# Optimization experiments

Hardware: AMD Instinct MI355X
Metric: run time of the kernel (lower is better)

The kernel has to match this reference:

```python
import jax, jax.numpy as jnp
import numpy as np

B, T, E, H = 1, 4096, 1024, 16
HD = E // H  # 64
SCALE = 8.0 / HD  # scaling='d' per Tensor Programs V


def setup_inputs() -> dict:
    key = jax.random.key(0)
    ks = jax.random.split(key, 7)
    s = 1.0 / np.sqrt(E)
    return {
        "q": jax.random.normal(ks[0], (B, T, E), jnp.float32),
        "k": jax.random.normal(ks[1], (B, T, E), jnp.float32),
        "v": jax.random.normal(ks[2], (B, T, E), jnp.float32),
        "Wq": jax.random.normal(ks[3], (E, E), jnp.float32) * s,
        "Wk": jax.random.normal(ks[4], (E, E), jnp.float32) * s,
        "Wv": jax.random.normal(ks[5], (E, E), jnp.float32) * s,
        "Wo": jax.random.normal(ks[6], (E, E), jnp.float32) * s,
    }


def reference(q, k, v, Wq, Wk, Wv, Wo):
    # bias-free linear projections (nn.Linear: y = x @ W.T)
    qp = q @ Wq.T
    kp = k @ Wk.T
    vp = v @ Wv.T
    # b t (h d) -> b h t d
    qh = qp.reshape(B, T, H, HD).transpose(0, 2, 1, 3)
    kh = kp.reshape(B, T, H, HD).transpose(0, 2, 1, 3)
    vh = vp.reshape(B, T, H, HD).transpose(0, 2, 1, 3)
    scores = jnp.einsum('bhqd,bhkd->bhqk', qh, kh) * SCALE
    # causal mask: positions k > q masked with -inf
    causal = jnp.tril(jnp.ones((T, T), dtype=bool))
    scores = jnp.where(causal[None, None], scores, -jnp.inf)
    probs = jax.nn.softmax(scores, axis=-1)
    out = jnp.einsum('bhqk,bhkd->bhqd', probs, vh)
    # b h t d -> b t (h d)
    out = out.transpose(0, 2, 1, 3).reshape(B, T, E)
    return out @ Wo.T
```

## Files before the change

kernel.cpp:

```cpp
#include <hip/hip_runtime.h>
#include <hip/hip_bf16.h>

#define T_DIM 4096
#define E_DIM 1024
#define H_DIM 16
#define HD_DIM 64
#define LOG2E_F 1.4426950408889634f
#define QSCALE_F (0.125f * LOG2E_F)

typedef __bf16 bf16_t;
typedef __bf16 bf16x8 __attribute__((ext_vector_type(8)));
typedef __bf16 bf16x4 __attribute__((ext_vector_type(4)));
typedef float  f32x4  __attribute__((ext_vector_type(4)));

__device__ inline void stage8(bf16_t* dst, const float* src) {
  const f32x4* s4 = (const f32x4*)src;
  f32x4 a = s4[0], b = s4[1];
  bf16x8 o;
  o[0] = (bf16_t)a[0]; o[1] = (bf16_t)a[1]; o[2] = (bf16_t)a[2]; o[3] = (bf16_t)a[3];
  o[4] = (bf16_t)b[0]; o[5] = (bf16_t)b[1]; o[6] = (bf16_t)b[2]; o[7] = (bf16_t)b[3];
  *(bf16x8*)dst = o;
}
__device__ inline void stage8(bf16_t* dst, const bf16_t* src) {
  *(bf16x8*)dst = *(const bf16x8*)src;
}

__device__ inline void gld_lds16(const bf16_t* g, bf16_t* l) {
  __builtin_amdgcn_global_load_lds(
      (const __attribute__((address_space(1))) unsigned int*)g,
      (__attribute__((address_space(3))) unsigned int*)l, 16, 0, 0);
}

__device__ inline float fexp2(float x) {
  float r;
  asm("v_exp_f32 %0, %1" : "=v"(r) : "v"(x));
  return r;
}

__device__ inline void block_sync() {
  asm volatile("" ::: "memory");
  __builtin_amdgcn_s_barrier();
  asm volatile("" ::: "memory");
}

__global__ __launch_bounds__(256) void cvt_all(
    const float* __restrict__ q, const float* __restrict__ k, const float* __restrict__ v,
    const float* __restrict__ Wq, const float* __restrict__ Wk,
    const float* __restrict__ Wv, const float* __restrict__ Wo,
    bf16_t* qb, bf16_t* kb, bf16_t* vb,
    bf16_t* Wqb, bf16_t* Wkb, bf16_t* Wvb, bf16_t* Wob) {
  for (int u = blockIdx.x * 256 + threadIdx.x; u < 2097152; u += gridDim.x * 256) {
    const float* s; bf16_t* d; int i;
    if (u < 1572864) {
      int seg = u >> 19, off = u & 524287;
      s = seg == 0 ? q : (seg == 1 ? k : v);
      d = seg == 0 ? qb : (seg == 1 ? kb : vb);
      i = off;
    } else {
      int w = u - 1572864;
      int seg = w >> 17, off = w & 131071;
      s = seg == 0 ? Wq : seg == 1 ? Wk : seg == 2 ? Wv : Wo;
      d = seg == 0 ? Wqb : seg == 1 ? Wkb : seg == 2 ? Wvb : Wob;
      i = off;
    }
    stage8(d + (size_t)i * 8, s + (size_t)i * 8);
  }
}

template <int MF, int NF, typename TC>
__device__ __forceinline__ void gemm_body(const bf16_t* __restrict__ A,
                                          const bf16_t* __restrict__ B,
                                          TC* __restrict__ C,
                                          int ldC, int bm, int bn, float cs) {
  constexpr int BM = 32 * MF, BN = 32 * NF;
  __shared__ alignas(16) bf16_t As[BM][64];
  __shared__ alignas(16) bf16_t Bs[BN][64];
  const int tid  = threadIdx.x;
  const int lane = tid & 63, w = tid >> 6;
  const int g = lane >> 4, l15 = lane & 15;
  const int wr = w >> 1, wc = w & 1;

  f32x4 acc[MF][NF] = {};

  for (int kt = 0; kt < 1024; kt += 64) {
    if (kt) __syncthreads();
#pragma unroll
    for (int p = 0; p < MF; ++p) {
      int s = p * 256 + tid;
      int row = s >> 3, c = s & 7;
      int cg = c ^ (row & 7);
      gld_lds16(&A[(size_t)(bm + row) * 1024 + kt + cg * 8], &As[0][0] + s * 8);
    }
#pragma unroll
    for (int p = 0; p < NF; ++p) {
      int s = p * 256 + tid;
      int row = s >> 3, c = s & 7;
      int cg = c ^ (row & 7);
      gld_lds16(&B[(size_t)(bn + row) * 1024 + kt + cg * 8], &Bs[0][0] + s * 8);
    }
    asm volatile("s_waitcnt vmcnt(0)" ::: "memory");
    __syncthreads();

#pragma unroll
    for (int hh = 0; hh < 2; ++hh) {
      bf16x8 af[MF], bfr[NF];
#pragma unroll
      for (int m = 0; m < MF; ++m) {
        int row = wr * (16 * MF) + m * 16 + l15;
        af[m] = *(const bf16x8*)(&As[0][0] + row * 64 + (((hh * 4 + g) ^ (row & 7)) * 8));
      }
#pragma unroll
      for (int n = 0; n < NF; ++n) {
        int row = wc * (16 * NF) + n * 16 + l15;
        bfr[n] = *(const bf16x8*)(&Bs[0][0] + row * 64 + (((hh * 4 + g) ^ (row & 7)) * 8));
      }
#pragma unroll
      for (int m = 0; m < MF; ++m)
#pragma unroll
        for (int n = 0; n < NF; ++n)
          acc[m][n] = __builtin_amdgcn_mfma_f32_16x16x32_bf16(af[m], bfr[n], acc[m][n], 0, 0, 0);
    }
  }

#pragma unroll
  for (int m = 0; m < MF; ++m)
#pragma unroll
    for (int n = 0; n < NF; ++n)
#pragma unroll
      for (int r = 0; r < 4; ++r) {
        int row = bm + wr * (16 * MF) + m * 16 + g * 4 + r;
        int col = bn + wc * (16 * NF) + n * 16 + l15;
        C[(size_t)row * ldC + col] = (TC)(acc[m][n][r] * cs);
      }
}

__global__ __launch_bounds__(256) void proj_qkv(
    const bf16_t* __restrict__ qb, const bf16_t* __restrict__ kb,
    const bf16_t* __restrict__ vb,
    const bf16_t* __restrict__ Wqb, const bf16_t* __restrict__ Wkb,
    const bf16_t* __restrict__ Wvb,
    bf16_t* Qp, bf16_t* Kp, bf16_t* Vt) {
  const int bid = blockIdx.x;
  const int which = bid >> 8, t = bid & 255;
  const bf16_t *A, *B; bf16_t* C; int ldC, bm, bn; float cs;
  if (which == 0) {
    A = qb;  B = Wqb; C = Qp; ldC = 1024;
    bm = (t >> 3) * 128; bn = (t & 7) * 128; cs = QSCALE_F;
  } else if (which == 1) {
    A = kb;  B = Wkb; C = Kp; ldC = 1024;
    bm = (t >> 3) * 128; bn = (t & 7) * 128; cs = 1.0f;
  } else {
    A = Wvb; B = vb;  C = Vt; ldC = 4096;
    bm = (t >> 5) * 128; bn = (t & 31) * 128; cs = 1.0f;
  }
  gemm_body<4, 4, bf16_t>(A, B, C, ldC, bm, bn, cs);
}

__global__ __launch_bounds__(256) void gemm_fin(const bf16_t* __restrict__ A,
                                                const bf16_t* __restrict__ B,
                                                float* __restrict__ C) {
  gemm_body<2, 4, float>(A, B, C, 1024, blockIdx.y * 64, blockIdx.x * 128, 1.0f);
}

template <typename TA, typename TB, typename TC>
__global__ __launch_bounds__(256) void gemm_bt(const TA* __restrict__ A,
                                               const TB* __restrict__ B,
                                               TC* __restrict__ C,
                                               int M, int N, int K, float cscale) {
  __shared__ alignas(16) bf16_t As[128][40];
  __shared__ alignas(16) bf16_t Bs[128][40];
  const int tid  = threadIdx.x;
  const int lane = tid & 63, w = tid >> 6;
  const int g = lane >> 4, l15 = lane & 15;
  const int wr = w >> 1, wc = w & 1;
  const int bm = blockIdx.y * 128, bn = blockIdx.x * 128;

  f32x4 acc[4][4] = {};

  for (int kt = 0; kt < K; kt += 32) {
    __syncthreads();
#pragma unroll
    for (int i = 0; i < 2; ++i) {
      int vv  = tid + i * 256;
      int row = vv >> 2, c8 = (vv & 3) * 8;
      stage8(&As[row][c8], &A[(size_t)(bm + row) * K + kt + c8]);
      stage8(&Bs[row][c8], &B[(size_t)(bn + row) * K + kt + c8]);
    }
    __syncthreads();

    bf16x8 af[4], bfr[4];
#pragma unroll
    for (int m = 0; m < 4; ++m)
      af[m] = *(const bf16x8*)&As[wr * 64 + m * 16 + l15][g * 8];
#pragma unroll
    for (int n = 0; n < 4; ++n)
      bfr[n] = *(const bf16x8*)&Bs[wc * 64 + n * 16 + l15][g * 8];
#pragma unroll
    for (int m = 0; m < 4; ++m)
#pragma unroll
      for (int n = 0; n < 4; ++n)
        acc[m][n] = __builtin_amdgcn_mfma_f32_16x16x32_bf16(af[m], bfr[n], acc[m][n], 0, 0, 0);
  }

#pragma unroll
  for (int m = 0; m < 4; ++m)
#pragma unroll
    for (int n = 0; n < 4; ++n)
#pragma unroll
      for (int r = 0; r < 4; ++r) {
        int row = bm + wr * 64 + m * 16 + g * 4 + r;
        int col = bn + wc * 64 + n * 16 + l15;
        C[(size_t)row * N + col] = (TC)(acc[m][n][r] * cscale);
      }
}

__global__ __launch_bounds__(256) void attn_fwd(const bf16_t* __restrict__ Qp,
                                                const bf16_t* __restrict__ Kp,
                                                const bf16_t* __restrict__ Vt,
                                                bf16_t* __restrict__ Oattn) {
  const int bid = blockIdx.x;
  const int h  = bid & 15;
  const int ii = bid >> 4;
  const int tid = threadIdx.x, lane = tid & 63, w = tid >> 6;
  const int g = lane >> 4, l15 = lane & 15;

  __shared__ alignas(16) bf16_t Ks[2][64][64];
  __shared__ alignas(16) bf16_t Vs[3][64][64];
  __shared__ alignas(16) bf16_t Plds[4][16][72];

  const int row0 = tid >> 3, c0 = tid & 7;
  const int cgo = (c0 ^ (row0 & 7)) * 8;
  const bf16_t* srcK0 = Kp + (size_t)row0 * E_DIM + h * 64 + cgo;
  const bf16_t* srcK1 = srcK0 + (size_t)32 * E_DIM;
  const bf16_t* srcV0 = Vt + (size_t)(h * 64 + row0) * T_DIM + cgo;
  const bf16_t* srcV1 = srcV0 + (size_t)32 * T_DIM;
  bf16_t* KsAll = &Ks[0][0][0];
  bf16_t* VsAll = &Vs[0][0][0];
  const size_t KADV = (size_t)64 * E_DIM;

  auto issue = [&](int t) {
    bf16_t* kd = KsAll + (t & 1) * 4096;
    bf16_t* vd = VsAll + (t % 3) * 4096;
    gld_lds16(srcK0 + (size_t)t * KADV, kd + tid * 8);
    gld_lds16(srcK1 + (size_t)t * KADV, kd + (256 + tid) * 8);
    gld_lds16(srcV0 + (size_t)t * 64,   vd + tid * 8);
    gld_lds16(srcV1 + (size_t)t * 64,   vd + (256 + tid) * 8);
  };

  f32x4 acc[4];
  float m_s, l_p;

  auto pv = [&](int t) {
    const char* Vb = (const char*)(VsAll + (t % 3) * 4096);
    bf16x8 pf0 = *(const bf16x8*)&Plds[w][l15][g * 8];
    bf16x8 pf1 = *(const bf16x8*)&Plds[w][l15][32 + g * 8];
#pragma unroll
    for (int c = 0; c < 4; ++c) {
      const int vr = c * 16 + l15;
      const char* rp = Vb + vr * 128;
      const int sw = (vr & 7) << 4;
      bf16x8 v0 = *(const bf16x8*)(rp + ((g * 16) ^ sw));
      bf16x8 v1 = *(const bf16x8*)(rp + ((64 + g * 16) ^ sw));
      acc[c] = __builtin_amdgcn_mfma_f32_16x16x32_bf16(v0, pf0, acc[c], 0, 0, 0);
      acc[c] = __builtin_amdgcn_mfma_f32_16x16x32_bf16(v1, pf1, acc[c], 0, 0, 0);
    }
  };

  for (int pass = 0; pass < 2; ++pass) {
    const int qi = pass ? ii : 63 - ii;
    const int qrow = qi * 64 + w * 16;
    const int nt = qi + 1;

    bf16x8 qf[2];
    {
      const bf16_t* qp = &Qp[(size_t)(qrow + l15) * E_DIM + h * 64 + g * 8];
      qf[0] = *(const bf16x8*)qp;
      qf[1] = *(const bf16x8*)(qp + 32);
    }
#pragma unroll
    for (int c = 0; c < 4; ++c)
#pragma unroll
      for (int r = 0; r < 4; ++r) acc[c][r] = 0.f;
    m_s = -1e30f; l_p = 0.f;

    if (pass) block_sync();
    issue(0);

    for (int j = 0; j < nt; ++j) {
      asm volatile("s_waitcnt vmcnt(0)" ::: "memory");
      block_sync();
      if (j + 1 < nt) issue(j + 1);

      __builtin_amdgcn_s_setprio(1);
      if (j > 0) pv(j - 1);

      const char* Kb = (const char*)(KsAll + (j & 1) * 4096);
      f32x4 s[4] = {};
#pragma unroll
      for (int j16 = 0; j16 < 4; ++j16) {
        const int r0 = j16 * 16 + l15;
        const char* rp = Kb + r0 * 128;
        const int sw = (r0 & 7) << 4;
        bf16x8 k0 = *(const bf16x8*)(rp + ((g * 16) ^ sw));
        bf16x8 k1 = *(const bf16x8*)(rp + ((64 + g * 16) ^ sw));
        s[j16] = __builtin_amdgcn_mfma_f32_16x16x32_bf16(k0, qf[0], s[j16], 0, 0, 0);
        s[j16] = __builtin_amdgcn_mfma_f32_16x16x32_bf16(k1, qf[1], s[j16], 0, 0, 0);
      }
      __builtin_amdgcn_s_setprio(0);

      if (j == nt - 1) {
        const int kb = j * 64;
#pragma unroll
        for (int j16 = 0; j16 < 4; ++j16)
#pragma unroll
          for (int r = 0; r < 4; ++r)
            if (kb + j16 * 16 + g * 4 + r > qrow + l15) s[j16][r] = -1e30f;
      }

      float pmax = s[0][0];
#pragma unroll
      for (int j16 = 0; j16 < 4; ++j16)
#pragma unroll
        for (int r = 0; r < 4; ++r) pmax = fmaxf(pmax, s[j16][r]);

      if (!__all(pmax <= m_s + 11.0f)) {
        float rm = fmaxf(pmax, __shfl_xor(pmax, 16));
        rm = fmaxf(rm, __shfl_xor(rm, 32));
        float mn = fmaxf(m_s, rm);
        float sc = fexp2(m_s - mn);
        m_s = mn;
        l_p *= sc;
#pragma unroll
        for (int c = 0; c < 4; ++c)
#pragma unroll
          for (int r = 0; r < 4; ++r) acc[c][r] *= sc;
      }

      float ps = 0.f;
#pragma unroll
      for (int j16 = 0; j16 < 4; ++j16)
#pragma unroll
        for (int r = 0; r < 4; ++r) {
          s[j16][r] = fexp2(s[j16][r] - m_s);
          ps += s[j16][r];
        }
      l_p += ps;

#pragma unroll
      for (int j16 = 0; j16 < 4; ++j16) {
        bf16x4 pk;
        pk[0] = (bf16_t)s[j16][0]; pk[1] = (bf16_t)s[j16][1];
        pk[2] = (bf16_t)s[j16][2]; pk[3] = (bf16_t)s[j16][3];
        *(bf16x4*)&Plds[w][l15][j16 * 16 + g * 4] = pk;
      }
    }

    pv(nt - 1);

    float lt = l_p;
    lt += __shfl_xor(lt, 16);
    lt += __shfl_xor(lt, 32);
    const float inv = 1.0f / lt;
#pragma unroll
    for (int c = 0; c < 4; ++c) {
      bf16x4 o;
#pragma unroll
      for (int r = 0; r < 4; ++r) o[r] = (bf16_t)(acc[c][r] * inv);
      *(bf16x4*)&Oattn[(size_t)(qrow + l15) * E_DIM + h * 64 + c * 16 + g * 4] = o;
    }
  }
}

extern "C" void kernel_launch(void* const* d_in, const int* in_sizes, int n_in,
                              void* d_out, int out_size, void* d_ws, size_t ws_size,
                              hipStream_t stream) {
  const float* q  = (const float*)d_in[0];
  const float* k  = (const float*)d_in[1];
  const float* v  = (const float*)d_in[2];
  const float* Wq = (const float*)d_in[3];
  const float* Wk = (const float*)d_in[4];
  const float* Wv = (const float*)d_in[5];
  const float* Wo = (const float*)d_in[6];
  float* out = (float*)d_out;

  const size_t TE = (size_t)T_DIM * E_DIM;
  const size_t EE = (size_t)E_DIM * E_DIM;
  dim3 blk(256);

  if (ws_size >= (size_t)56 * 1024 * 1024) {
    bf16_t* qb  = (bf16_t*)d_ws;
    bf16_t* kb  = qb + TE;
    bf16_t* vb  = kb + TE;
    bf16_t* Wqb = vb + TE;
    bf16_t* Wkb = Wqb + EE;
    bf16_t* Wvb = Wkb + EE;
    bf16_t* Wob = Wvb + EE;
    bf16_t* Qp  = Wob + EE;
    bf16_t* Kp  = Qp + TE;
    bf16_t* Vt  = Kp + TE;
    bf16_t* Oa  = qb;

    cvt_all<<<2048, blk, 0, stream>>>(q, k, v, Wq, Wk, Wv, Wo,
                                      qb, kb, vb, Wqb, Wkb, Wvb, Wob);
    proj_qkv<<<dim3(768), blk, 0, stream>>>(qb, kb, vb, Wqb, Wkb, Wvb, Qp, Kp, Vt);
    attn_fwd<<<dim3(512), blk, 0, stream>>>(Qp, Kp, Vt, Oa);
    gemm_fin<<<dim3(8, 64), blk, 0, stream>>>(Oa, Wob, out);
  } else {
    bf16_t* Qp = (bf16_t*)d_ws;
    bf16_t* Kp = Qp + TE;
    bf16_t* Vt = Kp + TE;
    bf16_t* Oa = Vt + TE;
    gemm_bt<float, float, bf16_t><<<dim3(8, 32), blk, 0, stream>>>(q, Wq, Qp, T_DIM, E_DIM, E_DIM, QSCALE_F);
    gemm_bt<float, float, bf16_t><<<dim3(8, 32), blk, 0, stream>>>(k, Wk, Kp, T_DIM, E_DIM, E_DIM, 1.0f);
    gemm_bt<float, float, bf16_t><<<dim3(32, 8), blk, 0, stream>>>(Wv, v, Vt, E_DIM, T_DIM, E_DIM, 1.0f);
    attn_fwd<<<dim3(512), blk, 0, stream>>>(Qp, Kp, Vt, Oa);
    gemm_bt<bf16_t, float, float><<<dim3(8, 32), blk, 0, stream>>>(Oa, Wo, out, T_DIM, E_DIM, E_DIM, 1.0f);
  }
}
```

Before: 131.6 us.

## Process two adjacent 64-row query tiles per block sharing each K/V tile

Each wave now carries two query row groups, 64 rows apart, within a 128-row block tile. Every K/V tile staged in shared memory feeds both groups' QK and PV MFMAs, which halves global K/V traffic per query row and doubles the independent MFMA work per sync. This replaces the old scheme that ran two mirrored 64-row tiles one after the other for load balance. The new mapping gives blocks uneven work (2 to 64 iterations), only partly offset by launching heavy blocks first. It also adds a fully masked extra tile for the first group and raises register pressure.

New measurement: 144.2 us. +9.6%, slower.

```diff
diff --git a/kernel.cpp b/kernel.cpp
--- a/kernel.cpp
+++ b/kernel.cpp
@@ -219,14 +219,27 @@
                                                 const bf16_t* __restrict__ Vt,
                                                 bf16_t* __restrict__ Oattn) {
   const int bid = blockIdx.x;
-  const int h  = bid & 15;
-  const int ii = bid >> 4;
+  const int h   = bid & 15;
+  const int idx = bid >> 4;
+  const int qi  = idx < 16 ? 31 - idx : idx - 16;
   const int tid = threadIdx.x, lane = tid & 63, w = tid >> 6;
   const int g = lane >> 4, l15 = lane & 15;
+  const int qrow_a = qi * 128 + w * 16;
+  const int qrow_b = qrow_a + 64;
 
   __shared__ alignas(16) bf16_t Ks[2][64][64];
   __shared__ alignas(16) bf16_t Vs[3][64][64];
-  __shared__ alignas(16) bf16_t Plds[4][16][72];
+  __shared__ alignas(16) bf16_t Plds[2][4][16][72];
+
+  bf16x8 qfa[2], qfb[2];
+  {
+    const bf16_t* qp = &Qp[(size_t)(qrow_a + l15) * E_DIM + h * 64 + g * 8];
+    qfa[0] = *(const bf16x8*)qp;
+    qfa[1] = *(const bf16x8*)(qp + 32);
+    const bf16_t* qp2 = qp + (size_t)64 * E_DIM;
+    qfb[0] = *(const bf16x8*)qp2;
+    qfb[1] = *(const bf16x8*)(qp2 + 32);
+  }
 
   const int row0 = tid >> 3, c0 = tid & 7;
   const int cgo = (c0 ^ (row0 & 7)) * 8;
@@ -237,6 +250,7 @@
   bf16_t* KsAll = &Ks[0][0][0];
   bf16_t* VsAll = &Vs[0][0][0];
   const size_t KADV = (size_t)64 * E_DIM;
+  const int nt = 2 * qi + 2;
 
   auto issue = [&](int t) {
     bf16_t* kd = KsAll + (t & 1) * 4096;
@@ -247,13 +261,16 @@
     gld_lds16(srcV1 + (size_t)t * 64,   vd + (256 + tid) * 8);
   };
 
-  f32x4 acc[4];
-  float m_s, l_p;
+  f32x4 acca[4] = {}, accb[4] = {};
+  float m_a = -1e30f, l_a = 0.f;
+  float m_b = -1e30f, l_b = 0.f;
 
   auto pv = [&](int t) {
     const char* Vb = (const char*)(VsAll + (t % 3) * 4096);
-    bf16x8 pf0 = *(const bf16x8*)&Plds[w][l15][g * 8];
-    bf16x8 pf1 = *(const bf16x8*)&Plds[w][l15][32 + g * 8];
+    bf16x8 pa0 = *(const bf16x8*)&Plds[0][w][l15][g * 8];
+    bf16x8 pa1 = *(const bf16x8*)&Plds[0][w][l15][32 + g * 8];
+    bf16x8 pb0 = *(const bf16x8*)&Plds[1][w][l15][g * 8];
+    bf16x8 pb1 = *(const bf16x8*)&Plds[1][w][l15][32 + g * 8];
 #pragma unroll
     for (int c = 0; c < 4; ++c) {
       const int vr = c * 16 + l15;
@@ -261,113 +278,115 @@
       const int sw = (vr & 7) << 4;
       bf16x8 v0 = *(const bf16x8*)(rp + ((g * 16) ^ sw));
       bf16x8 v1 = *(const bf16x8*)(rp + ((64 + g * 16) ^ sw));
-      acc[c] = __builtin_amdgcn_mfma_f32_16x16x32_bf16(v0, pf0, acc[c], 0, 0, 0);
-      acc[c] = __builtin_amdgcn_mfma_f32_16x16x32_bf16(v1, pf1, acc[c], 0, 0, 0);
+      acca[c] = __builtin_amdgcn_mfma_f32_16x16x32_bf16(v0, pa0, acca[c], 0, 0, 0);
+      acca[c] = __builtin_amdgcn_mfma_f32_16x16x32_bf16(v1, pa1, acca[c], 0, 0, 0);
+      accb[c] = __builtin_amdgcn_mfma_f32_16x16x32_bf16(v0, pb0, accb[c], 0, 0, 0);
+      accb[c] = __builtin_amdgcn_mfma_f32_16x16x32_bf16(v1, pb1, accb[c], 0, 0, 0);
     }
   };
 
-  for (int pass = 0; pass < 2; ++pass) {
-    const int qi = pass ? ii : 63 - ii;
-    const int qrow = qi * 64 + w * 16;
-    const int nt = qi + 1;
-
-    bf16x8 qf[2];
-    {
-      const bf16_t* qp = &Qp[(size_t)(qrow + l15) * E_DIM + h * 64 + g * 8];
-      qf[0] = *(const bf16x8*)qp;
-      qf[1] = *(const bf16x8*)(qp + 32);
-    }
-#pragma unroll
-    for (int c = 0; c < 4; ++c)
-#pragma unroll
-      for (int r = 0; r < 4; ++r) acc[c][r] = 0.f;
-    m_s = -1e30f; l_p = 0.f;
-
-    if (pass) block_sync();
-    issue(0);
-
-    for (int j = 0; j < nt; ++j) {
-      asm volatile("s_waitcnt vmcnt(0)" ::: "memory");
-      block_sync();
-      if (j + 1 < nt) issue(j + 1);
-
-      __builtin_amdgcn_s_setprio(1);
-      if (j > 0) pv(j - 1);
-
-      const char* Kb = (const char*)(KsAll + (j & 1) * 4096);
-      f32x4 s[4] = {};
-#pragma unroll
-      for (int j16 = 0; j16 < 4; ++j16) {
-        const int r0 = j16 * 16 + l15;
-        const char* rp = Kb + r0 * 128;
-        const int sw = (r0 & 7) << 4;
-        bf16x8 k0 = *(const bf16x8*)(rp + ((g * 16) ^ sw));
-        bf16x8 k1 = *(const bf16x8*)(rp + ((64 + g * 16) ^ sw));
-        s[j16] = __builtin_amdgcn_mfma_f32_16x16x32_bf16(k0, qf[0], s[j16], 0, 0, 0);
-        s[j16] = __builtin_amdgcn_mfma_f32_16x16x32_bf16(k1, qf[1], s[j16], 0, 0, 0);
+  auto softmax_p = [&](f32x4 (&s)[4], float& m_s, float& l_p, f32x4 (&acc)[4],
+                       int grp) {
+    float pmax = s[0][0];
+#pragma unroll
+    for (int j16 = 0; j16 < 4; ++j16)
+#pragma unroll
+      for (int r = 0; r < 4; ++r) pmax = fmaxf(pmax, s[j16][r]);
+
+    if (!__all(pmax <= m_s + 11.0f)) {
+      float rm = fmaxf(pmax, __shfl_xor(pmax, 16));
+      rm = fmaxf(rm, __shfl_xor(rm, 32));
+      float mn = fmaxf(m_s, rm);
+      float sc = fexp2(m_s - mn);
+      m_s = mn;
+      l_p *= sc;
+#pragma unroll
+      for (int c = 0; c < 4; ++c)
+#pragma unroll
+        for (int r = 0; r < 4; ++r) acc[c][r] *= sc;
+    }
+
+    float ps = 0.f;
+#pragma unroll
+    for (int j16 = 0; j16 < 4; ++j16)
+#pragma unroll
+      for (int r = 0; r < 4; ++r) {
+        s[j16][r] = fexp2(s[j16][r] - m_s);
+        ps += s[j16][r];
       }
-      __builtin_amdgcn_s_setprio(0);
-
-      if (j == nt - 1) {
-        const int kb = j * 64;
-#pragma unroll
-        for (int j16 = 0; j16 < 4; ++j16)
-#pragma unroll
-          for (int r = 0; r < 4; ++r)
-            if (kb + j16 * 16 + g * 4 + r > qrow + l15) s[j16][r] = -1e30f;
-      }
-
-      float pmax = s[0][0];
+    l_p += ps;
+
+#pragma unroll
+    for (int j16 = 0; j16 < 4; ++j16) {
+      bf16x4 pk;
+      pk[0] = (bf16_t)s[j16][0]; pk[1] = (bf16_t)s[j16][1];
+      pk[2] = (bf16_t)s[j16][2]; pk[3] = (bf16_t)s[j16][3];
+      *(bf16x4*)&Plds[grp][w][l15][j16 * 16 + g * 4] = pk;
+    }
+  };
+
+  issue(0);
+
+  for (int j = 0; j < nt; ++j) {
+    asm volatile("s_waitcnt vmcnt(0)" ::: "memory");
+    block_sync();
+    if (j + 1 < nt) issue(j + 1);
+
+    __builtin_amdgcn_s_setprio(1);
+    if (j > 0) pv(j - 1);
+
+    const char* Kb = (const char*)(KsAll + (j & 1) * 4096);
+    f32x4 sa[4] = {}, sb[4] = {};
+#pragma unroll
+    for (int j16 = 0; j16 < 4; ++j16) {
+      const int r0 = j16 * 16 + l15;
+      const char* rp = Kb + r0 * 128;
+      const int sw = (r0 & 7) << 4;
+      bf16x8 k0 = *(const bf16x8*)(rp + ((g * 16) ^ sw));
+      bf16x8 k1 = *(const bf16x8*)(rp + ((64 + g * 16) ^ sw));
+      sa[j16] = __builtin_amdgcn_mfma_f32_16x16x32_bf16(k0, qfa[0], sa[j16], 0, 0, 0);
+      sa[j16] = __builtin_amdgcn_mfma_f32_16x16x32_bf16(k1, qfa[1], sa[j16], 0, 0, 0);
+      sb[j16] = __builtin_amdgcn_mfma_f32_16x16x32_bf16(k0, qfb[0], sb[j16], 0, 0, 0);
+      sb[j16] = __builtin_amdgcn_mfma_f32_16x16x32_bf16(k1, qfb[1], sb[j16], 0, 0, 0);
+    }
+    __builtin_amdgcn_s_setprio(0);
+
+    const int kb = j * 64;
+    if (kb + 63 > qrow_a) {
 #pragma unroll
       for (int j16 = 0; j16 < 4; ++j16)
 #pragma unroll
-        for (int r = 0; r < 4; ++r) pmax = fmaxf(pmax, s[j16][r]);
-
-      if (!__all(pmax <= m_s + 11.0f)) {
-        float rm = fmaxf(pmax, __shfl_xor(pmax, 16));
-        rm = fmaxf(rm, __shfl_xor(rm, 32));
-        float mn = fmaxf(m_s, rm);
-        float sc = fexp2(m_s - mn);
-        m_s = mn;
-        l_p *= sc;
-#pragma unroll
-        for (int c = 0; c < 4; ++c)
-#pragma unroll
-          for (int r = 0; r < 4; ++r) acc[c][r] *= sc;
-      }
-
-      float ps = 0.f;
+        for (int r = 0; r < 4; ++r)
+          if (kb + j16 * 16 + g * 4 + r > qrow_a + l15) sa[j16][r] = -1e30f;
+    }
+    if (kb + 63 > qrow_b) {
 #pragma unroll
       for (int j16 = 0; j16 < 4; ++j16)
 #pragma unroll
-        for (int r = 0; r < 4; ++r) {
-          s[j16][r] = fexp2(s[j16][r] - m_s);
-          ps += s[j16][r];
-        }
-      l_p += ps;
-
-#pragma unroll
-      for (int j16 = 0; j16 < 4; ++j16) {
-        bf16x4 pk;
-        pk[0] = (bf16_t)s[j16][0]; pk[1] = (bf16_t)s[j16][1];
-        pk[2] = (bf16_t)s[j16][2]; pk[3] = (bf16_t)s[j16][3];
-        *(bf16x4*)&Plds[w][l15][j16 * 16 + g * 4] = pk;
-      }
-    }
-
-    pv(nt - 1);
-
-    float lt = l_p;
-    lt += __shfl_xor(lt, 16);
-    lt += __shfl_xor(lt, 32);
-    const float inv = 1.0f / lt;
-#pragma unroll
-    for (int c = 0; c < 4; ++c) {
-      bf16x4 o;
-#pragma unroll
-      for (int r = 0; r < 4; ++r) o[r] = (bf16_t)(acc[c][r] * inv);
-      *(bf16x4*)&Oattn[(size_t)(qrow + l15) * E_DIM + h * 64 + c * 16 + g * 4] = o;
-    }
+        for (int r = 0; r < 4; ++r)
+          if (kb + j16 * 16 + g * 4 + r > qrow_b + l15) sb[j16][r] = -1e30f;
+    }
+
+    softmax_p(sa, m_a, l_a, acca, 0);
+    softmax_p(sb, m_b, l_b, accb, 1);
+  }
+
+  pv(nt - 1);
+
+  float la = l_a, lb = l_b;
+  la += __shfl_xor(la, 16); la += __shfl_xor(la, 32);
+  lb += __shfl_xor(lb, 16); lb += __shfl_xor(lb, 32);
+  const float inva = 1.0f / la, invb = 1.0f / lb;
+#pragma unroll
+  for (int c = 0; c < 4; ++c) {
+    bf16x4 oa, ob;
+#pragma unroll
+    for (int r = 0; r < 4; ++r) {
+      oa[r] = (bf16_t)(acca[c][r] * inva);
+      ob[r] = (bf16_t)(accb[c][r] * invb);
+    }
+    *(bf16x4*)&Oattn[(size_t)(qrow_a + l15) * E_DIM + h * 64 + c * 16 + g * 4] = oa;
+    *(bf16x4*)&Oattn[(size_t)(qrow_b + l15) * E_DIM + h * 64 + c * 16 + g * 4] = ob;
   }
 }
 
```

## Use 512-thread attention blocks covering 128 query rows, dropping two-pass pairing

Applied to the files above, without the earlier changes.

The attention kernel now launches 8 waves per block, each block handling a 128-row query tile instead of two 64-row tiles in sequence. Every K/V tile loaded into LDS is shared by twice as many waves, so each thread issues half as many global-to-LDS copies. Load balance now comes from an ordering of query tiles with the heaviest causal tiles first, replacing the pairing of light and heavy tiles in one block. The causal mask is applied to any tile crossing the diagonal rather than only the last one. The risks are idle waves on the diagonal tiles, uneven work per block, and lower occupancy from larger blocks.

New measurement: 126.2 us. -4.1%, faster.

```diff
diff --git a/kernel.cpp b/kernel.cpp
--- a/kernel.cpp
+++ b/kernel.cpp
@@ -214,41 +214,45 @@
       }
 }
 
-__global__ __launch_bounds__(256) void attn_fwd(const bf16_t* __restrict__ Qp,
+__global__ __launch_bounds__(512) void attn_fwd(const bf16_t* __restrict__ Qp,
                                                 const bf16_t* __restrict__ Kp,
                                                 const bf16_t* __restrict__ Vt,
                                                 bf16_t* __restrict__ Oattn) {
   const int bid = blockIdx.x;
-  const int h  = bid & 15;
-  const int ii = bid >> 4;
+  const int h   = bid & 15;
+  const int idx = bid >> 4;
+  const int qi  = idx < 16 ? 31 - idx : idx - 16;
   const int tid = threadIdx.x, lane = tid & 63, w = tid >> 6;
   const int g = lane >> 4, l15 = lane & 15;
+  const int qrow = qi * 128 + w * 16;
 
   __shared__ alignas(16) bf16_t Ks[2][64][64];
   __shared__ alignas(16) bf16_t Vs[3][64][64];
-  __shared__ alignas(16) bf16_t Plds[4][16][72];
+  __shared__ alignas(16) bf16_t Plds[8][16][72];
+
+  bf16x8 qf[2];
+  {
+    const bf16_t* qp = &Qp[(size_t)(qrow + l15) * E_DIM + h * 64 + g * 8];
+    qf[0] = *(const bf16x8*)qp;
+    qf[1] = *(const bf16x8*)(qp + 32);
+  }
 
   const int row0 = tid >> 3, c0 = tid & 7;
   const int cgo = (c0 ^ (row0 & 7)) * 8;
-  const bf16_t* srcK0 = Kp + (size_t)row0 * E_DIM + h * 64 + cgo;
-  const bf16_t* srcK1 = srcK0 + (size_t)32 * E_DIM;
-  const bf16_t* srcV0 = Vt + (size_t)(h * 64 + row0) * T_DIM + cgo;
-  const bf16_t* srcV1 = srcV0 + (size_t)32 * T_DIM;
+  const bf16_t* srcK = Kp + (size_t)row0 * E_DIM + h * 64 + cgo;
+  const bf16_t* srcV = Vt + (size_t)(h * 64 + row0) * T_DIM + cgo;
   bf16_t* KsAll = &Ks[0][0][0];
   bf16_t* VsAll = &Vs[0][0][0];
   const size_t KADV = (size_t)64 * E_DIM;
+  const int nt = 2 * qi + 2;
 
   auto issue = [&](int t) {
-    bf16_t* kd = KsAll + (t & 1) * 4096;
-    bf16_t* vd = VsAll + (t % 3) * 4096;
-    gld_lds16(srcK0 + (size_t)t * KADV, kd + tid * 8);
-    gld_lds16(srcK1 + (size_t)t * KADV, kd + (256 + tid) * 8);
-    gld_lds16(srcV0 + (size_t)t * 64,   vd + tid * 8);
-    gld_lds16(srcV1 + (size_t)t * 64,   vd + (256 + tid) * 8);
+    gld_lds16(srcK + (size_t)t * KADV, KsAll + (t & 1) * 4096 + tid * 8);
+    gld_lds16(srcV + (size_t)t * 64,   VsAll + (t % 3) * 4096 + tid * 8);
   };
 
-  f32x4 acc[4];
-  float m_s, l_p;
+  f32x4 acc[4] = {};
+  float m_s = -1e30f, l_p = 0.f;
 
   auto pv = [&](int t) {
     const char* Vb = (const char*)(VsAll + (t % 3) * 4096);
@@ -266,108 +270,89 @@
     }
   };
 
-  for (int pass = 0; pass < 2; ++pass) {
-    const int qi = pass ? ii : 63 - ii;
-    const int qrow = qi * 64 + w * 16;
-    const int nt = qi + 1;
-
-    bf16x8 qf[2];
-    {
-      const bf16_t* qp = &Qp[(size_t)(qrow + l15) * E_DIM + h * 64 + g * 8];
-      qf[0] = *(const bf16x8*)qp;
-      qf[1] = *(const bf16x8*)(qp + 32);
-    }
-#pragma unroll
-    for (int c = 0; c < 4; ++c)
-#pragma unroll
-      for (int r = 0; r < 4; ++r) acc[c][r] = 0.f;
-    m_s = -1e30f; l_p = 0.f;
-
-    if (pass) block_sync();
-    issue(0);
-
-    for (int j = 0; j < nt; ++j) {
-      asm volatile("s_waitcnt vmcnt(0)" ::: "memory");
-      block_sync();
-      if (j + 1 < nt) issue(j + 1);
-
-      __builtin_amdgcn_s_setprio(1);
-      if (j > 0) pv(j - 1);
-
-      const char* Kb = (const char*)(KsAll + (j & 1) * 4096);
-      f32x4 s[4] = {};
-#pragma unroll
-      for (int j16 = 0; j16 < 4; ++j16) {
-        const int r0 = j16 * 16 + l15;
-        const char* rp = Kb + r0 * 128;
-        const int sw = (r0 & 7) << 4;
-        bf16x8 k0 = *(const bf16x8*)(rp + ((g * 16) ^ sw));
-        bf16x8 k1 = *(const bf16x8*)(rp + ((64 + g * 16) ^ sw));
-        s[j16] = __builtin_amdgcn_mfma_f32_16x16x32_bf16(k0, qf[0], s[j16], 0, 0, 0);
-        s[j16] = __builtin_amdgcn_mfma_f32_16x16x32_bf16(k1, qf[1], s[j16], 0, 0, 0);
+  issue(0);
+
+  for (int j = 0; j < nt; ++j) {
+    asm volatile("s_waitcnt vmcnt(0)" ::: "memory");
+    block_sync();
+    if (j + 1 < nt) issue(j + 1);
+
+    __builtin_amdgcn_s_setprio(1);
+    if (j > 0) pv(j - 1);
+
+    const char* Kb = (const char*)(KsAll + (j & 1) * 4096);
+    f32x4 s[4] = {};
+#pragma unroll
+    for (int j16 = 0; j16 < 4; ++j16) {
+      const int r0 = j16 * 16 + l15;
+      const char* rp = Kb + r0 * 128;
+      const int sw = (r0 & 7) << 4;
+      bf16x8 k0 = *(const bf16x8*)(rp + ((g * 16) ^ sw));
+      bf16x8 k1 = *(const bf16x8*)(rp + ((64 + g * 16) ^ sw));
+      s[j16] = __builtin_amdgcn_mfma_f32_16x16x32_bf16(k0, qf[0], s[j16], 0, 0, 0);
+      s[j16] = __builtin_amdgcn_mfma_f32_16x16x32_bf16(k1, qf[1], s[j16], 0, 0, 0);
+    }
+    __builtin_amdgcn_s_setprio(0);
+
+    const int kb = j * 64;
+    if (kb + 63 > qrow) {
+#pragma unroll
+      for (int j16 = 0; j16 < 4; ++j16)
+#pragma unroll
+        for (int r = 0; r < 4; ++r)
+          if (kb + j16 * 16 + g * 4 + r > qrow + l15) s[j16][r] = -1e30f;
+    }
+
+    float pmax = s[0][0];
+#pragma unroll
+    for (int j16 = 0; j16 < 4; ++j16)
+#pragma unroll
+      for (int r = 0; r < 4; ++r) pmax = fmaxf(pmax, s[j16][r]);
+
+    if (!__all(pmax <= m_s + 11.0f)) {
+      float rm = fmaxf(pmax, __shfl_xor(pmax, 16));
+      rm = fmaxf(rm, __shfl_xor(rm, 32));
+      float mn = fmaxf(m_s, rm);
+      float sc = fexp2(m_s - mn);
+      m_s = mn;
+      l_p *= sc;
+#pragma unroll
+      for (int c = 0; c < 4; ++c)
+#pragma unroll
+        for (int r = 0; r < 4; ++r) acc[c][r] *= sc;
+    }
+
+    float ps = 0.f;
+#pragma unroll
+    for (int j16 = 0; j16 < 4; ++j16)
+#pragma unroll
+      for (int r = 0; r < 4; ++r) {
+        s[j16][r] = fexp2(s[j16][r] - m_s);
+        ps += s[j16][r];
       }
-      __builtin_amdgcn_s_setprio(0);
-
-      if (j == nt - 1) {
-        const int kb = j * 64;
-#pragma unroll
-        for (int j16 = 0; j16 < 4; ++j16)
-#pragma unroll
-          for (int r = 0; r < 4; ++r)
-            if (kb + j16 * 16 + g * 4 + r > qrow + l15) s[j16][r] = -1e30f;
-      }
-
-      float pmax = s[0][0];
-#pragma unroll
-      for (int j16 = 0; j16 < 4; ++j16)
-#pragma unroll
-        for (int r = 0; r < 4; ++r) pmax = fmaxf(pmax, s[j16][r]);
-
-      if (!__all(pmax <= m_s + 11.0f)) {
-        float rm = fmaxf(pmax, __shfl_xor(pmax, 16));
-        rm = fmaxf(rm, __shfl_xor(rm, 32));
-        float mn = fmaxf(m_s, rm);
-        float sc = fexp2(m_s - mn);
-        m_s = mn;
-        l_p *= sc;
-#pragma unroll
-        for (int c = 0; c < 4; ++c)
-#pragma unroll
-          for (int r = 0; r < 4; ++r) acc[c][r] *= sc;
-      }
-
-      float ps = 0.f;
-#pragma unroll
-      for (int j16 = 0; j16 < 4; ++j16)
-#pragma unroll
-        for (int r = 0; r < 4; ++r) {
-          s[j16][r] = fexp2(s[j16][r] - m_s);
-          ps += s[j16][r];
-        }
-      l_p += ps;
-
-#pragma unroll
-      for (int j16 = 0; j16 < 4; ++j16) {
-        bf16x4 pk;
-        pk[0] = (bf16_t)s[j16][0]; pk[1] = (bf16_t)s[j16][1];
-        pk[2] = (bf16_t)s[j16][2]; pk[3] = (bf16_t)s[j16][3];
-        *(bf16x4*)&Plds[w][l15][j16 * 16 + g * 4] = pk;
-      }
-    }
-
-    pv(nt - 1);
-
-    float lt = l_p;
-    lt += __shfl_xor(lt, 16);
-    lt += __shfl_xor(lt, 32);
-    const float inv = 1.0f / lt;
-#pragma unroll
-    for (int c = 0; c < 4; ++c) {
-      bf16x4 o;
-#pragma unroll
-      for (int r = 0; r < 4; ++r) o[r] = (bf16_t)(acc[c][r] * inv);
-      *(bf16x4*)&Oattn[(size_t)(qrow + l15) * E_DIM + h * 64 + c * 16 + g * 4] = o;
-    }
+    l_p += ps;
+
+#pragma unroll
+    for (int j16 = 0; j16 < 4; ++j16) {
+      bf16x4 pk;
+      pk[0] = (bf16_t)s[j16][0]; pk[1] = (bf16_t)s[j16][1];
+      pk[2] = (bf16_t)s[j16][2]; pk[3] = (bf16_t)s[j16][3];
+      *(bf16x4*)&Plds[w][l15][j16 * 16 + g * 4] = pk;
+    }
+  }
+
+  pv(nt - 1);
+
+  float lt = l_p;
+  lt += __shfl_xor(lt, 16);
+  lt += __shfl_xor(lt, 32);
+  const float inv = 1.0f / lt;
+#pragma unroll
+  for (int c = 0; c < 4; ++c) {
+    bf16x4 o;
+#pragma unroll
+    for (int r = 0; r < 4; ++r) o[r] = (bf16_t)(acc[c][r] * inv);
+    *(bf16x4*)&Oattn[(size_t)(qrow + l15) * E_DIM + h * 64 + c * 16 + g * 4] = o;
   }
 }
 
@@ -403,7 +388,7 @@
     cvt_all<<<2048, blk, 0, stream>>>(q, k, v, Wq, Wk, Wv, Wo,
                                       qb, kb, vb, Wqb, Wkb, Wvb, Wob);
     proj_qkv<<<dim3(768), blk, 0, stream>>>(qb, kb, vb, Wqb, Wkb, Wvb, Qp, Kp, Vt);
-    attn_fwd<<<dim3(512), blk, 0, stream>>>(Qp, Kp, Vt, Oa);
+    attn_fwd<<<dim3(512), dim3(512), 0, stream>>>(Qp, Kp, Vt, Oa);
     gemm_fin<<<dim3(8, 64), blk, 0, stream>>>(Oa, Wob, out);
   } else {
     bf16_t* Qp = (bf16_t*)d_ws;
@@ -413,7 +398,7 @@
     gemm_bt<float, float, bf16_t><<<dim3(8, 32), blk, 0, stream>>>(q, Wq, Qp, T_DIM, E_DIM, E_DIM, QSCALE_F);
     gemm_bt<float, float, bf16_t><<<dim3(8, 32), blk, 0, stream>>>(k, Wk, Kp, T_DIM, E_DIM, E_DIM, 1.0f);
     gemm_bt<float, float, bf16_t><<<dim3(32, 8), blk, 0, stream>>>(Wv, v, Vt, E_DIM, T_DIM, E_DIM, 1.0f);
-    attn_fwd<<<dim3(512), blk, 0, stream>>>(Qp, Kp, Vt, Oa);
+    attn_fwd<<<dim3(512), dim3(512), 0, stream>>>(Qp, Kp, Vt, Oa);
     gemm_bt<bf16_t, float, float><<<dim3(8, 32), blk, 0, stream>>>(Oa, Wo, out, T_DIM, E_DIM, E_DIM, 1.0f);
   }
 }
```
